# Kernel tuning notes

Measured on AMD Instinct MI355X. Metric: run time of the kernel, lower is better.

The kernel has to match this reference:

```python
import jax, jax.numpy as jnp
import numpy as np

B, S, D, H, DFF = 2, 2048, 1024, 16, 4096
DH = D // H
EPS = 1e-5


def setup_inputs() -> dict:
    key = jax.random.key(0)
    ks = jax.random.split(key, 12)
    s = 0.02
    x = jax.random.normal(ks[0], (B, S, D), dtype=jnp.float32)
    # causal decoder mask, True = keep
    mask = jnp.tril(jnp.ones((S, S), dtype=bool))[None, None, :, :]
    Wq = jax.random.normal(ks[1], (D, D), dtype=jnp.float32) * s
    Wk = jax.random.normal(ks[2], (D, D), dtype=jnp.float32) * s
    Wv = jax.random.normal(ks[3], (D, D), dtype=jnp.float32) * s
    Wo = jax.random.normal(ks[4], (D, D), dtype=jnp.float32) * s
    w1 = jax.random.normal(ks[5], (D, DFF), dtype=jnp.float32) * s
    b1 = jnp.zeros((DFF,), dtype=jnp.float32)
    w2 = jax.random.normal(ks[6], (DFF, D), dtype=jnp.float32) * s
    b2 = jnp.zeros((D,), dtype=jnp.float32)
    g1 = jnp.ones((D,), dtype=jnp.float32)
    be1 = jnp.zeros((D,), dtype=jnp.float32)
    g2 = jnp.ones((D,), dtype=jnp.float32)
    be2 = jnp.zeros((D,), dtype=jnp.float32)
    return dict(x=x, mask=mask, Wq=Wq, Wk=Wk, Wv=Wv, Wo=Wo,
                w1=w1, b1=b1, w2=w2, b2=b2, g1=g1, be1=be1, g2=g2, be2=be2)


def _layer_norm(x, gamma, beta):
    mu = jnp.mean(x, axis=-1, keepdims=True)
    var = jnp.mean(jnp.square(x - mu), axis=-1, keepdims=True)
    return (x - mu) * jax.lax.rsqrt(var + EPS) * gamma + beta


def _attention(x, mask, Wq, Wk, Wv, Wo):
    # x: [B,S,D] -> q,k,v: [B,H,S,DH]
    def split_heads(t):
        return t.reshape(x.shape[0], x.shape[1], H, DH).transpose(0, 2, 1, 3)
    q = split_heads(x @ Wq)
    k = split_heads(x @ Wk)
    v = split_heads(x @ Wv)
    scores = jnp.einsum('bhqd,bhkd->bhqk', q, k) / jnp.sqrt(jnp.float32(DH))
    scores = jnp.where(mask, scores, jnp.float32(-1e9))
    probs = jax.nn.softmax(scores, axis=-1)
    out = jnp.einsum('bhqk,bhkd->bhqd', probs, v)  # [B,H,S,DH]
    out = out.transpose(0, 2, 1, 3).reshape(x.shape[0], x.shape[1], -1)
    return out @ Wo


def reference(x, mask, Wq, Wk, Wv, Wo, w1, b1, w2, b2, g1, be1, g2, be2):
    # residual 1: pre-norm self-attention (dropout=0)
    h = x + _attention(_layer_norm(x, g1, be1), mask, Wq, Wk, Wv, Wo)
    # residual 2: pre-norm FFN
    hn = _layer_norm(h, g2, be2)
    ffn = jax.nn.relu(hn @ w1 + b1) @ w2 + b2
    return h + ffn
```

## Files before the change

### kernel.cpp

```cpp
#include <hip/hip_runtime.h>

typedef unsigned short u16;
typedef __attribute__((ext_vector_type(8))) short short8;
typedef __attribute__((ext_vector_type(4))) float f32x4;

#define CB 2
#define CS 2048
#define CD 1024
#define CH 16
#define CDH 64
#define CDFF 4096
#define NQB (CS / 64)

__device__ __forceinline__ u16 f2bf(float f){
  union { float f; unsigned u; } x; x.f = f;
  unsigned r = (x.u + 0x7fffu + ((x.u >> 16) & 1u)) >> 16;
  return (u16)r;
}

__device__ __forceinline__ u16 f2bf_pos(float f){
  union { float f; unsigned u; } x; x.f = f;
  return (u16)((x.u + 0x8000u) >> 16);
}

__device__ __forceinline__ void gload_lds16(const void* g, void* l){
  __builtin_amdgcn_global_load_lds(
    (const __attribute__((address_space(1))) void*)(unsigned long long)g,
    (__attribute__((address_space(3))) void*)(unsigned long long)l,
    16, 0, 0);
}

struct TPAll { const float* s[6]; u16* d[6]; };

__global__ __launch_bounds__(256)
void transpose_all(TPAll p)
{
  __shared__ float t[32][33];
  const int g = blockIdx.x >> 12;
  const int id = blockIdx.x & 4095;
  const float* __restrict__ in;
  u16* __restrict__ out;
  int K, N, n0, k0;
  if (g == 0){
    const int w = id >> 10, tile = id & 1023;
    in = p.s[w]; out = p.d[w]; K = 1024; N = 1024;
    n0 = (tile & 31) * 32; k0 = (tile >> 5) * 32;
  } else if (g == 1){
    in = p.s[4]; out = p.d[4]; K = 1024; N = 4096;
    n0 = (id & 127) * 32; k0 = (id >> 7) * 32;
  } else {
    in = p.s[5]; out = p.d[5]; K = 4096; N = 1024;
    n0 = (id & 31) * 32; k0 = (id >> 5) * 32;
  }
  const int c = threadIdx.x & 31, r4 = threadIdx.x >> 5;
  #pragma unroll
  for (int i = 0; i < 4; i++){
    int r = r4 + i * 8;
    t[r][c] = in[(size_t)(k0 + r) * N + n0 + c];
  }
  __syncthreads();
  #pragma unroll
  for (int i = 0; i < 4; i++){
    int r = r4 + i * 8;
    out[(size_t)(n0 + r) * K + k0 + c] = f2bf(t[c][r]);
  }
}

template<int MODE>
__global__ __launch_bounds__(256)
void ln_bf16(const float* __restrict__ xin, const float* __restrict__ g,
             const float* __restrict__ be, u16* __restrict__ outp,
             float4* __restrict__ aux, const float* __restrict__ bias)
{
  const int row = blockIdx.x, tid = threadIdx.x;
  const int lane = tid & 63, wave = tid >> 6;
  const float4 v = ((const float4*)(xin + (size_t)row * CD))[tid];
  float s  = v.x + v.y + v.z + v.w;
  float s2 = v.x*v.x + v.y*v.y + v.z*v.z + v.w*v.w;
  #pragma unroll
  for (int m = 1; m < 64; m <<= 1){ s += __shfl_xor(s, m); s2 += __shfl_xor(s2, m); }
  __shared__ float red[8];
  if (lane == 0){ red[wave] = s; red[4 + wave] = s2; }

  if (MODE == 2){
    const float4 b4 = ((const float4*)bias)[tid];
    float4 w = v;
    w.x += b4.x; w.y += b4.y; w.z += b4.z; w.w += b4.w;
    aux[(size_t)row * 256 + tid] = w;
  }

  __syncthreads();
  s  = red[0] + red[1] + red[2] + red[3];
  s2 = red[4] + red[5] + red[6] + red[7];
  const float mu = s * (1.0f / CD);
  const float var = s2 * (1.0f / CD) - mu * mu;
  const float rs = rsqrtf(var + 1e-5f);
  const float4 gv = ((const float4*)g)[tid];
  const float4 bv = ((const float4*)be)[tid];
  ushort4 o;
  o.x = f2bf((v.x - mu) * rs * gv.x + bv.x);
  o.y = f2bf((v.y - mu) * rs * gv.y + bv.y);
  o.z = f2bf((v.z - mu) * rs * gv.z + bv.z);
  o.w = f2bf((v.w - mu) * rs * gv.w + bv.w);
  ((ushort4*)outp)[(size_t)row * (CD / 4) + tid] = o;
}

template<int EPI>
__global__ __launch_bounds__(256)
void gemm_bt(const u16* __restrict__ A, const u16* __restrict__ Bt,
             void* __restrict__ Cout, const float* __restrict__ bias,
             int M, int N, int K,
             int ldc, int vsplit, u16* __restrict__ vtout)
{
  __shared__ __align__(16) u16 lA[128 * 64];
  __shared__ __align__(16) u16 lB[128 * 64];
  const int tid = threadIdx.x;
  const int wave = tid >> 6, lane = tid & 63;

  const int G = gridDim.x;
  const int flat = blockIdx.x;
  const int t = (flat & 7) * (G >> 3) + (flat >> 3);
  const int NN = N >> 7;
  const int n_i = t % NN;
  const int m_i = t / NN;

  const int m0 = m_i * 128, n0 = n_i * 128;
  const int wm = (wave >> 1) * 64, wn = (wave & 1) * 64;
  const int lq = lane >> 4, lr = lane & 15;

  f32x4 acc[4][4] = {};

  const u16* Ab = A + (size_t)m0 * K;
  const u16* Bb = Bt + (size_t)n0 * K;
  const int srow = lane >> 3;
  const int scol = (lane & 7) * 8;

  for (int k0 = 0; k0 < K; k0 += 64){
    __syncthreads();
    #pragma unroll
    for (int i = 0; i < 4; i++){
      const int c = i * 4 + wave;
      const int row = c * 8 + srow;
      gload_lds16(Ab + (size_t)row * K + k0 + scol, &lA[c * 512]);
      gload_lds16(Bb + (size_t)row * K + k0 + scol, &lB[c * 512]);
    }
    __syncthreads();
    #pragma unroll
    for (int kk = 0; kk < 64; kk += 32){
      short8 aF[4], bF[4];
      #pragma unroll
      for (int i = 0; i < 4; i++) aF[i] = *(const short8*)&lA[(wm + i * 16 + lr) * 64 + kk + lq * 8];
      #pragma unroll
      for (int j = 0; j < 4; j++) bF[j] = *(const short8*)&lB[(wn + j * 16 + lr) * 64 + kk + lq * 8];
      #pragma unroll
      for (int i = 0; i < 4; i++)
        #pragma unroll
        for (int j = 0; j < 4; j++)
          acc[i][j] = __builtin_amdgcn_mfma_f32_16x16x32_bf16(aF[i], bF[j], acc[i][j], 0, 0, 0);
    }
  }

  if (EPI == 0 && n0 >= vsplit){
    #pragma unroll
    for (int i = 0; i < 4; i++){
      const int row0 = m0 + wm + i * 16 + lq * 4;
      const int bb = row0 >> 11, s = row0 & 2047;
      #pragma unroll
      for (int j = 0; j < 4; j++){
        const int col = n0 - vsplit + wn + j * 16 + lr;
        ushort4 o;
        o.x = f2bf(acc[i][j][0]); o.y = f2bf(acc[i][j][1]);
        o.z = f2bf(acc[i][j][2]); o.w = f2bf(acc[i][j][3]);
        *(ushort4*)&vtout[((size_t)(bb * 1024 + col)) * CS + s] = o;
      }
    }
    return;
  }

  const float osc = (EPI == 0 && n0 < 1024) ? 0.125f : 1.0f;

  #pragma unroll
  for (int i = 0; i < 4; i++){
    const int row = m0 + wm + i * 16 + lq * 4;
    #pragma unroll
    for (int j = 0; j < 4; j++){
      const int col = n0 + wn + j * 16 + lr;
      #pragma unroll
      for (int r = 0; r < 4; r++){
        float v = acc[i][j][r];
        const size_t off = (size_t)(row + r) * ldc + col;
        if (EPI == 0){
          ((u16*)Cout)[off] = f2bf(v * osc);
        } else {
          v += bias[col]; v = v > 0.0f ? v : 0.0f;
          ((u16*)Cout)[off] = f2bf(v);
        }
      }
    }
  }
}

__global__ __launch_bounds__(256)
void gemm_bt64(const u16* __restrict__ A, const u16* __restrict__ Bt,
               const float* __restrict__ resid, float* __restrict__ Cout,
               int M, int N, int K)
{
  __shared__ __align__(16) u16 lA[2][64 * 64];
  __shared__ __align__(16) u16 lB[2][128 * 64];
  const int tid = threadIdx.x;
  const int wave = tid >> 6, lane = tid & 63;

  const int G = gridDim.x;
  const int flat = blockIdx.x;
  const int t = (flat & 7) * (G >> 3) + (flat >> 3);
  const int NN = N >> 7;
  const int n_i = t % NN;
  const int m_i = t / NN;
  const int m0 = m_i * 64, n0 = n_i * 128;
  const int lq = lane >> 4, lr = lane & 15;

  f32x4 acc[4][2] = {};

  const u16* Ab = A + (size_t)m0 * K;
  const u16* Bb = Bt + (size_t)n0 * K;
  const int srow = lane >> 3, scol = (lane & 7) * 8;

  auto stage = [&](int buf, int kt){
    const int k0 = kt * 64;
    #pragma unroll
    for (int i = 0; i < 6; i++){
      const int c = i * 4 + wave;
      if (c < 8){
        gload_lds16(Ab + (size_t)(c * 8 + srow) * K + k0 + scol, &lA[buf][c * 512]);
      } else {
        const int cb2 = c - 8;
        gload_lds16(Bb + (size_t)(cb2 * 8 + srow) * K + k0 + scol, &lB[buf][cb2 * 512]);
      }
    }
  };

  const int nit = K >> 6;
  stage(0, 0);
  for (int i = 0; i < nit; i++){
    const int cb = i & 1;
    if (i + 1 < nit){
      stage(cb ^ 1, i + 1);
      asm volatile("s_waitcnt vmcnt(6)\n\ts_barrier" ::: "memory");
    } else {
      asm volatile("s_waitcnt vmcnt(0)\n\ts_barrier" ::: "memory");
    }
    #pragma unroll
    for (int kk = 0; kk < 64; kk += 32){
      short8 aF[4], bF[2];
      #pragma unroll
      for (int i2 = 0; i2 < 4; i2++) aF[i2] = *(const short8*)&lA[cb][(i2 * 16 + lr) * 64 + kk + lq * 8];
      #pragma unroll
      for (int j = 0; j < 2; j++) bF[j] = *(const short8*)&lB[cb][(wave * 32 + j * 16 + lr) * 64 + kk + lq * 8];
      #pragma unroll
      for (int i2 = 0; i2 < 4; i2++)
        #pragma unroll
        for (int j = 0; j < 2; j++)
          acc[i2][j] = __builtin_amdgcn_mfma_f32_16x16x32_bf16(aF[i2], bF[j], acc[i2][j], 0, 0, 0);
    }
    asm volatile("s_barrier" ::: "memory");
  }

  #pragma unroll
  for (int i = 0; i < 4; i++){
    const int row = m0 + i * 16 + lq * 4;
    #pragma unroll
    for (int j = 0; j < 2; j++){
      const int col = n0 + wave * 32 + j * 16 + lr;
      #pragma unroll
      for (int r = 0; r < 4; r++){
        const size_t off = (size_t)(row + r) * N + col;
        Cout[off] = resid[off] + acc[i][j][r];
      }
    }
  }
}

__global__ __launch_bounds__(256)
void attn_kernel(const u16* __restrict__ qk, const u16* __restrict__ vt,
                 u16* __restrict__ outp)
{
  __shared__ __align__(16) u16 lK[2][64 * 64];
  __shared__ __align__(16) u16 lVt[2][64 * 64];
  __shared__ __align__(16) u16 lP[4][16 * 72];
  const int tid = threadIdx.x, wave = tid >> 6, lane = tid & 63;
  const int lq = lane >> 4, lr = lane & 15;
  const int bh = blockIdx.x, b = bh >> 4, h = bh & 15;
  const int RS = 2048;
  const int srow = lane >> 3, scol = (lane & 7) * 8;

  const size_t kbase = (size_t)(b * CS) * RS + 1024 + h * CDH;
  const size_t vbase = (size_t)(bh * CDH) * CS;
  u16* lPw = lP[wave];

  auto stageKV = [&](int buf, int kt){
    #pragma unroll
    for (int cc = 0; cc < 2; cc++){
      const int c = wave * 2 + cc;
      gload_lds16(qk + kbase + (size_t)(kt * 64 + c * 8 + srow) * RS + scol, &lK[buf][c * 512]);
      gload_lds16(vt + vbase + (size_t)(c * 8 + srow) * CS + kt * 64 + scol, &lVt[buf][c * 512]);
    }
  };

  #pragma unroll 1
  for (int part = 0; part < 2; part++){
    const int iq = part ? (NQB - 1 - blockIdx.y) : blockIdx.y;
    const int q0 = iq * 64;
    const int ktmax = iq + 1;

    const int qrow = b * CS + q0 + wave * 16 + lr;
    const u16* qp = qk + (size_t)qrow * RS + h * CDH;
    const short8 qf0 = *(const short8*)(qp + lq * 8);
    const short8 qf1 = *(const short8*)(qp + 32 + lq * 8);

    f32x4 o[4] = {};
    float lsum[4] = {0.0f, 0.0f, 0.0f, 0.0f};

    stageKV(0, 0);
    for (int kt = 0; kt < ktmax; ++kt){
      const int cb = kt & 1;
      if (kt + 1 < ktmax){
        stageKV(cb ^ 1, kt + 1);
        asm volatile("s_waitcnt vmcnt(4)\n\ts_barrier" ::: "memory");
      } else {
        asm volatile("s_waitcnt vmcnt(0)\n\ts_barrier" ::: "memory");
      }

      f32x4 s[4] = {};
      #pragma unroll
      for (int nb = 0; nb < 4; nb++){
        const short8 bk0 = *(const short8*)&lK[cb][(nb * 16 + lr) * 64 + lq * 8];
        const short8 bk1 = *(const short8*)&lK[cb][(nb * 16 + lr) * 64 + 32 + lq * 8];
        s[nb] = __builtin_amdgcn_mfma_f32_16x16x32_bf16(qf0, bk0, s[nb], 0, 0, 0);
        s[nb] = __builtin_amdgcn_mfma_f32_16x16x32_bf16(qf1, bk1, s[nb], 0, 0, 0);
      }

      const bool diag = (kt + 1) == ktmax;
      const int qg = q0 + wave * 16 + lq * 4;
      #pragma unroll
      for (int r = 0; r < 4; r++){
        float e0 = __expf(s[0][r]);
        float e1 = __expf(s[1][r]);
        float e2 = __expf(s[2][r]);
        float e3 = __expf(s[3][r]);
        if (diag){
          const int q = qg + r, kb = kt * 64 + lr;
          e0 = (kb      <= q) ? e0 : 0.0f;
          e1 = (kb + 16 <= q) ? e1 : 0.0f;
          e2 = (kb + 32 <= q) ? e2 : 0.0f;
          e3 = (kb + 48 <= q) ? e3 : 0.0f;
        }
        lsum[r] += (e0 + e1) + (e2 + e3);
        const int prow = (lq * 4 + r) * 72;
        lPw[prow + lr]      = f2bf_pos(e0);
        lPw[prow + 16 + lr] = f2bf_pos(e1);
        lPw[prow + 32 + lr] = f2bf_pos(e2);
        lPw[prow + 48 + lr] = f2bf_pos(e3);
      }

      asm volatile("s_waitcnt lgkmcnt(0)" ::: "memory");
      const short8 pf0 = *(const short8*)&lPw[lr * 72 + lq * 8];
      const short8 pf1 = *(const short8*)&lPw[lr * 72 + 32 + lq * 8];

      #pragma unroll
      for (int nb = 0; nb < 4; nb++){
        const short8 bv0 = *(const short8*)&lVt[cb][(nb * 16 + lr) * 64 + lq * 8];
        const short8 bv1 = *(const short8*)&lVt[cb][(nb * 16 + lr) * 64 + 32 + lq * 8];
        o[nb] = __builtin_amdgcn_mfma_f32_16x16x32_bf16(pf0, bv0, o[nb], 0, 0, 0);
        o[nb] = __builtin_amdgcn_mfma_f32_16x16x32_bf16(pf1, bv1, o[nb], 0, 0, 0);
      }
      asm volatile("s_barrier" ::: "memory");
    }

    #pragma unroll
    for (int r = 0; r < 4; r++){
      float l = lsum[r];
      l += __shfl_xor(l, 1);
      l += __shfl_xor(l, 2);
      l += __shfl_xor(l, 4);
      l += __shfl_xor(l, 8);
      const float inv = __builtin_amdgcn_rcpf(l);
      const size_t row = (size_t)(b * CS + q0 + wave * 16 + lq * 4 + r);
      #pragma unroll
      for (int nb = 0; nb < 4; nb++)
        outp[row * CD + h * CDH + nb * 16 + lr] = f2bf(o[nb][r] * inv);
    }
  }
}

extern "C" void kernel_launch(void* const* d_in, const int* in_sizes, int n_in,
                              void* d_out, int out_size, void* d_ws, size_t ws_size,
                              hipStream_t stream)
{
  const float* x   = (const float*)d_in[0];
  const float* Wq  = (const float*)d_in[2];
  const float* Wk  = (const float*)d_in[3];
  const float* Wv  = (const float*)d_in[4];
  const float* Wo  = (const float*)d_in[5];
  const float* w1  = (const float*)d_in[6];
  const float* b1  = (const float*)d_in[7];
  const float* w2  = (const float*)d_in[8];
  const float* b2  = (const float*)d_in[9];
  const float* g1  = (const float*)d_in[10];
  const float* be1 = (const float*)d_in[11];
  const float* g2  = (const float*)d_in[12];
  const float* be2 = (const float*)d_in[13];
  float* out = (float*)d_out;

  char* ws = (char*)d_ws;
  const size_t MB = 1u << 20;
  u16* yln    = (u16*)(ws);
  u16* qk     = (u16*)(ws + 8  * MB);
  u16* vt     = (u16*)(ws + 24 * MB);
  u16* attn   = (u16*)(ws + 32 * MB);
  u16* mid    = (u16*)(ws + 40 * MB);
  u16* Wqkv_t = (u16*)(ws + 72 * MB);
  u16* Wo_t   = (u16*)(ws + 78 * MB);
  u16* w1_t   = (u16*)(ws + 80 * MB);
  u16* w2_t   = (u16*)(ws + 88 * MB);

  const int M = CB * CS;
  const int BIG = 1 << 30;

  TPAll pa;
  pa.s[0] = Wq; pa.s[1] = Wk; pa.s[2] = Wv; pa.s[3] = Wo; pa.s[4] = w1; pa.s[5] = w2;
  pa.d[0] = Wqkv_t;
  pa.d[1] = Wqkv_t + (size_t)CD * CD;
  pa.d[2] = Wqkv_t + (size_t)2 * CD * CD;
  pa.d[3] = Wo_t;
  pa.d[4] = w1_t;
  pa.d[5] = w2_t;
  transpose_all<<<3 * 4096, 256, 0, stream>>>(pa);

  ln_bf16<0><<<M, 256, 0, stream>>>(x, g1, be1, yln, nullptr, nullptr);
  gemm_bt<0><<<24 * 32, 256, 0, stream>>>(yln, Wqkv_t, qk, nullptr, M, 3 * CD, CD, 2048, 2048, vt);
  attn_kernel<<<dim3(CB * CH, NQB / 2), 256, 0, stream>>>(qk, vt, attn);
  gemm_bt64<<<64 * 8, 256, 0, stream>>>(attn, Wo_t, x, out, M, CD, CD);
  ln_bf16<2><<<M, 256, 0, stream>>>(out, g2, be2, yln, (float4*)out, b2);
  gemm_bt<1><<<32 * 32, 256, 0, stream>>>(yln, w1_t, mid, b1, M, CDFF, CD, CDFF, BIG, nullptr);
  gemm_bt64<<<64 * 8, 256, 0, stream>>>(mid, w2_t, out, out, M, CD, CDFF);
}
```

Measured before the change: 382.6 us.

## Double-buffer LDS in gemm_bt and fuse first layernorm into weight-prep kernel

Splits the gemm_bt LDS tiles into two buffers, so the global-to-LDS load for the next K step is issued before computing the current one, with explicit vmcnt waits and barriers. This hides global load latency behind MFMA work. It doubles LDS use to 64KB per block, which may lower occupancy. Separately, the first LayerNorm is folded into the weight transpose launch as an extra block group, removing one kernel launch.

```diff
diff --git a/kernel.cpp b/kernel.cpp
--- a/kernel.cpp
+++ b/kernel.cpp
@@ -33,11 +33,41 @@
 struct TPAll { const float* s[6]; u16* d[6]; };
 
 __global__ __launch_bounds__(256)
-void transpose_all(TPAll p)
-{
-  __shared__ float t[32][33];
+void prep_all(TPAll p, const float* __restrict__ x, const float* __restrict__ g1,
+              const float* __restrict__ be1, u16* __restrict__ yln)
+{
   const int g = blockIdx.x >> 12;
   const int id = blockIdx.x & 4095;
+  const int tid = threadIdx.x;
+
+  if (g == 3){
+    const int row = id;
+    const int lane = tid & 63, wave = tid >> 6;
+    const float4 v = ((const float4*)(x + (size_t)row * CD))[tid];
+    float s  = v.x + v.y + v.z + v.w;
+    float s2 = v.x*v.x + v.y*v.y + v.z*v.z + v.w*v.w;
+    #pragma unroll
+    for (int m = 1; m < 64; m <<= 1){ s += __shfl_xor(s, m); s2 += __shfl_xor(s2, m); }
+    __shared__ float red[8];
+    if (lane == 0){ red[wave] = s; red[4 + wave] = s2; }
+    __syncthreads();
+    s  = red[0] + red[1] + red[2] + red[3];
+    s2 = red[4] + red[5] + red[6] + red[7];
+    const float mu = s * (1.0f / CD);
+    const float var = s2 * (1.0f / CD) - mu * mu;
+    const float rs = rsqrtf(var + 1e-5f);
+    const float4 gv = ((const float4*)g1)[tid];
+    const float4 bv = ((const float4*)be1)[tid];
+    ushort4 o;
+    o.x = f2bf((v.x - mu) * rs * gv.x + bv.x);
+    o.y = f2bf((v.y - mu) * rs * gv.y + bv.y);
+    o.z = f2bf((v.z - mu) * rs * gv.z + bv.z);
+    o.w = f2bf((v.w - mu) * rs * gv.w + bv.w);
+    ((ushort4*)yln)[(size_t)row * (CD / 4) + tid] = o;
+    return;
+  }
+
+  __shared__ float t[32][33];
   const float* __restrict__ in;
   u16* __restrict__ out;
   int K, N, n0, k0;
@@ -52,7 +82,7 @@
     in = p.s[5]; out = p.d[5]; K = 4096; N = 1024;
     n0 = (id & 31) * 32; k0 = (id >> 5) * 32;
   }
-  const int c = threadIdx.x & 31, r4 = threadIdx.x >> 5;
+  const int c = tid & 31, r4 = tid >> 5;
   #pragma unroll
   for (int i = 0; i < 4; i++){
     int r = r4 + i * 8;
@@ -112,8 +142,8 @@
              int M, int N, int K,
              int ldc, int vsplit, u16* __restrict__ vtout)
 {
-  __shared__ __align__(16) u16 lA[128 * 64];
-  __shared__ __align__(16) u16 lB[128 * 64];
+  __shared__ __align__(16) u16 lA[2][128 * 64];
+  __shared__ __align__(16) u16 lB[2][128 * 64];
   const int tid = threadIdx.x;
   const int wave = tid >> 6, lane = tid & 63;
 
@@ -135,29 +165,40 @@
   const int srow = lane >> 3;
   const int scol = (lane & 7) * 8;
 
-  for (int k0 = 0; k0 < K; k0 += 64){
-    __syncthreads();
+  auto stage = [&](int buf, int k0){
     #pragma unroll
     for (int i = 0; i < 4; i++){
       const int c = i * 4 + wave;
       const int row = c * 8 + srow;
-      gload_lds16(Ab + (size_t)row * K + k0 + scol, &lA[c * 512]);
-      gload_lds16(Bb + (size_t)row * K + k0 + scol, &lB[c * 512]);
-    }
-    __syncthreads();
+      gload_lds16(Ab + (size_t)row * K + k0 + scol, &lA[buf][c * 512]);
+      gload_lds16(Bb + (size_t)row * K + k0 + scol, &lB[buf][c * 512]);
+    }
+  };
+
+  const int nit = K >> 6;
+  stage(0, 0);
+  for (int i = 0; i < nit; i++){
+    const int cb = i & 1;
+    if (i + 1 < nit){
+      stage(cb ^ 1, (i + 1) * 64);
+      asm volatile("s_waitcnt vmcnt(8)\n\ts_barrier" ::: "memory");
+    } else {
+      asm volatile("s_waitcnt vmcnt(0)\n\ts_barrier" ::: "memory");
+    }
     #pragma unroll
     for (int kk = 0; kk < 64; kk += 32){
       short8 aF[4], bF[4];
       #pragma unroll
-      for (int i = 0; i < 4; i++) aF[i] = *(const short8*)&lA[(wm + i * 16 + lr) * 64 + kk + lq * 8];
-      #pragma unroll
-      for (int j = 0; j < 4; j++) bF[j] = *(const short8*)&lB[(wn + j * 16 + lr) * 64 + kk + lq * 8];
-      #pragma unroll
-      for (int i = 0; i < 4; i++)
+      for (int i2 = 0; i2 < 4; i2++) aF[i2] = *(const short8*)&lA[cb][(wm + i2 * 16 + lr) * 64 + kk + lq * 8];
+      #pragma unroll
+      for (int j = 0; j < 4; j++) bF[j] = *(const short8*)&lB[cb][(wn + j * 16 + lr) * 64 + kk + lq * 8];
+      #pragma unroll
+      for (int i2 = 0; i2 < 4; i2++)
         #pragma unroll
         for (int j = 0; j < 4; j++)
-          acc[i][j] = __builtin_amdgcn_mfma_f32_16x16x32_bf16(aF[i], bF[j], acc[i][j], 0, 0, 0);
-    }
+          acc[i2][j] = __builtin_amdgcn_mfma_f32_16x16x32_bf16(aF[i2], bF[j], acc[i2][j], 0, 0, 0);
+    }
+    asm volatile("s_barrier" ::: "memory");
   }
 
   if (EPI == 0 && n0 >= vsplit){
@@ -434,9 +475,8 @@
   pa.d[3] = Wo_t;
   pa.d[4] = w1_t;
   pa.d[5] = w2_t;
-  transpose_all<<<3 * 4096, 256, 0, stream>>>(pa);
-
-  ln_bf16<0><<<M, 256, 0, stream>>>(x, g1, be1, yln, nullptr, nullptr);
+  prep_all<<<4 * 4096, 256, 0, stream>>>(pa, x, g1, be1, yln);
+
   gemm_bt<0><<<24 * 32, 256, 0, stream>>>(yln, Wqkv_t, qk, nullptr, M, 3 * CD, CD, 2048, 2048, vt);
   attn_kernel<<<dim3(CB * CH, NQB / 2), 256, 0, stream>>>(qk, vt, attn);
   gemm_bt64<<<64 * 8, 256, 0, stream>>>(attn, Wo_t, x, out, M, CD, CD);
```

Result: faster. 355.9 us (-7.0%).
